# Kernel optimization log

Hardware: AMD Instinct MI355X
Metric: run time of the kernel (lower is better)

Reference implementation:

```python
import jax, jax.numpy as jnp
import numpy as np
from jax import lax

DIM = 96
B, S = 2, 48
EPS_LN = 1e-6
EPS_GRN = 1e-6


def setup_inputs() -> dict:
    key = jax.random.key(0)
    ks = jax.random.split(key, 11)
    d, h = DIM, 4 * DIM
    return {
        "x": jax.random.normal(ks[0], (B, d, S, S, S), jnp.float32),
        "dw_w": jax.random.normal(ks[1], (d, 1, 7, 7, 7), jnp.float32) * 0.05,  # (O, I/groups, kD,kH,kW)
        "dw_b": jax.random.normal(ks[2], (d,), jnp.float32) * 0.02,
        "ln_w": jnp.ones((d,), jnp.float32),
        "ln_b": jnp.zeros((d,), jnp.float32),
        "w1": jax.random.normal(ks[3], (d, h), jnp.float32) * 0.02,
        "b1": jax.random.normal(ks[4], (h,), jnp.float32) * 0.02,
        "grn_w": jax.random.normal(ks[5], (h,), jnp.float32) * 0.02,
        "grn_b": jax.random.normal(ks[6], (h,), jnp.float32) * 0.02,
        "w2": jax.random.normal(ks[7], (h, d), jnp.float32) * 0.02,
        "b2": jax.random.normal(ks[8], (d,), jnp.float32) * 0.02,
    }


def reference(x, dw_w, dw_b, ln_w, ln_b, w1, b1, grn_w, grn_b, w2, b2):
    # depthwise 7x7x7 conv, padding 3, groups = channels; x: (B, C, D, H, W)
    y = lax.conv_general_dilated(
        x, dw_w, window_strides=(1, 1, 1), padding=[(3, 3)] * 3,
        dimension_numbers=("NCDHW", "OIDHW", "NCDHW"), feature_group_count=DIM,
    ) + dw_b[None, :, None, None, None]
    # channels_last: (B, D, H, W, C)
    h = jnp.transpose(y, (0, 2, 3, 4, 1))
    # LayerNorm over channel dim
    mu = jnp.mean(h, axis=-1, keepdims=True)
    var = jnp.mean((h - mu) ** 2, axis=-1, keepdims=True)
    h = (h - mu) * lax.rsqrt(var + EPS_LN) * ln_w + ln_b
    # pointwise MLP expand + GELU (exact, erf-based, like torch)
    h = jnp.einsum("bdhwc,ce->bdhwe", h, w1) + b1
    h = jax.nn.gelu(h, approximate=False)
    # GRN: global L2 norm over spatial dims (1,2,3), per channel
    g = jnp.sqrt(jnp.sum(h * h, axis=(1, 2, 3), keepdims=True))  # (B,1,1,1,4C)
    n = g / (jnp.mean(g, axis=-1, keepdims=True) + EPS_GRN)
    h = grn_w * (h * n) + grn_b + h
    # pointwise MLP contract
    h = jnp.einsum("bdhwe,ec->bdhwc", h, w2) + b2
    # back to channels_first + residual
    return x + jnp.transpose(h, (0, 4, 1, 2, 3))
```

## Files before the change

### kernel.cpp

```cpp
#include <hip/hip_runtime.h>
#include <hip/hip_bf16.h>
#include <string.h>

#define S3 110592
#define CDIM 96
#define EDIM 384
#define ZIN 14
#define YIN 22

typedef __attribute__((ext_vector_type(8))) short bf16x8;
typedef __attribute__((ext_vector_type(4))) float f32x4;
typedef unsigned short ushort_t;

__device__ __forceinline__ ushort_t f2bf(float f) {
  __hip_bfloat16 h = __float2bfloat16(f);
  union { __hip_bfloat16 h; ushort_t u; } cv; cv.h = h; return cv.u;
}
__device__ __forceinline__ float bf2f(ushort_t u) {
  union { __hip_bfloat16 h; ushort_t u; } cv; cv.u = u; return __bfloat162float(cv.h);
}

__global__ void kprep(const float* __restrict__ ln_w, const float* __restrict__ ln_b,
                      const float* __restrict__ w1, const float* __restrict__ b1,
                      const float* __restrict__ grn_b, const float* __restrict__ w2,
                      const float* __restrict__ b2,
                      ushort_t* __restrict__ w1p, float* __restrict__ b1f, float* __restrict__ bias2) {
  int idx = blockIdx.x * 256 + threadIdx.x;
  if (idx < 24 * 3 * 64 * 8) {
    int j = idx & 7, lane = (idx >> 3) & 63, ks = (idx >> 9) % 3, nt = idx / 1536;
    int c = ks * 32 + (lane >> 4) * 8 + j;
    int e = nt * 16 + (lane & 15);
    w1p[idx] = f2bf(ln_w[c] * w1[c * EDIM + e]);
  }
  if (idx < EDIM) {
    float s = b1[idx];
    for (int c = 0; c < CDIM; ++c) s += ln_b[c] * w1[c * EDIM + idx];
    b1f[idx] = s;
  }
  if (idx < CDIM) {
    float s = b2[idx];
    for (int e = 0; e < EDIM; ++e) s += grn_b[e] * w2[e * CDIM + idx];
    bias2[idx] = s;
  }
}

__global__ void kpackB(const float* __restrict__ dw_w, ushort_t* __restrict__ Btab) {
  int idx = blockIdx.x * 256 + threadIdx.x;
  if (idx >= 96 * 49 * 512) return;
  int pos = idx & 511; int t = (idx >> 9) % 49; int c = idx / (49 * 512);
  int lane = pos >> 3, j = pos & 7;
  int k = (lane >> 4) * 8 + j, n = lane & 15;
  int tx = k - n - 1;
  int tz = t / 7, ty = t % 7;
  float v = (tx >= 0 && tx < 7) ? dw_w[c * 343 + tz * 49 + ty * 7 + tx] : 0.f;
  Btab[idx] = f2bf(v);
}

template<int HALF>
__device__ __forceinline__ void conv_ty_loop(const unsigned* tile, const ushort_t* Bt,
                                             int lane, int am, int xg, f32x4* acc) {
#pragma unroll 1
  for (int ty = 0; ty < 7; ++ty) {
    bf16x8 bfr[7];
#pragma unroll
    for (int tz = 0; tz < 7; ++tz)
      bfr[tz] = *(const bf16x8*)&Bt[(tz * 7 + ty) * 512 + lane * 8];
    int rowbase = am + ty;
#pragma unroll
    for (int zl = 0; zl < 7; ++zl) {
      int row = (HALF * 7 + zl) * YIN + rowbase;
      int byteoff = (row << 7) + (xg ^ ((row & 7) << 4));
      bf16x8 af = *(const bf16x8*)((const char*)tile + byteoff);
#pragma unroll
      for (int tz = 0; tz < 7; ++tz) {
        int l = (HALF == 0) ? (zl - tz) : (zl + 6 - tz);
        if (l >= 0 && l < 7)
          acc[l] = __builtin_amdgcn_mfma_f32_16x16x32_bf16(af, bfr[tz], acc[l], 0, 0, 0);
      }
    }
  }
}

__global__ __launch_bounds__(384, 6) void kconv(const float* __restrict__ x,
                                                const ushort_t* __restrict__ Btab,
                                                const float* __restrict__ dw_b,
                                                ushort_t* __restrict__ y) {
  __shared__ unsigned tile[ZIN * YIN * 32];
  int bid = blockIdx.x;
  int yt = bid % 3, zt = (bid / 3) % 6, bc = bid / 18;
  int c = bc % 96;
  int z0 = zt * 8, y0 = yt * 16;
  size_t base = (size_t)bc * S3;
  int tid = threadIdx.x;

  for (int i = tid; i < 308 * 8; i += 384) {
    int row = i >> 3; int pe = i & 7;
    int pc = (pe < 2) ? pe : pe + 24;
    tile[(row << 5) + (pc ^ ((row & 7) << 2))] = 0u;
  }
#pragma unroll 4
  for (int i = tid; i < 308 * 24; i += 384) {
    int row = i / 24; int pc = 2 + (i - row * 24);
    int dz = row / YIN, dy = row - dz * YIN;
    int gz = z0 - 3 + dz, gy = y0 - 3 + dy;
    float2 v = make_float2(0.f, 0.f);
    if ((unsigned)gz < 48u && (unsigned)gy < 48u)
      v = *(const float2*)&x[base + (size_t)gz * 2304 + gy * 48 + 2 * pc - 4];
    tile[(row << 5) + (pc ^ ((row & 7) << 2))] = (unsigned)f2bf(v.x) | ((unsigned)f2bf(v.y) << 16);
  }
  __syncthreads();

  int w = tid >> 6;
  int X = w % 3, half = w / 3;
  int lane = tid & 63;
  int am = lane & 15, g = lane >> 4;
  int xg = X * 32 + g * 16;

  f32x4 acc[7];
#pragma unroll
  for (int p = 0; p < 7; ++p) acc[p] = (f32x4){0.f, 0.f, 0.f, 0.f};

  const ushort_t* __restrict__ Bt = Btab + (size_t)c * 49 * 512;
  if (half == 0) conv_ty_loop<0>(tile, Bt, lane, am, xg, acc);
  else           conv_ty_loop<1>(tile, Bt, lane, am, xg, acc);

  float bv = dw_b[c];
  float* red = (float*)tile;
  int rcol = X * 16 + am;
  __syncthreads();
  if (half == 0) {
#pragma unroll
    for (int l = 1; l < 7; ++l)
#pragma unroll
      for (int r = 0; r < 4; ++r)
        red[(l - 1) * 800 + (g * 4 + r) * 50 + rcol] = acc[l][r];
  }
  __syncthreads();
  if (half == 0) {
    size_t zb = base + (size_t)z0 * 2304;
#pragma unroll
    for (int r = 0; r < 4; ++r)
      y[zb + (size_t)(y0 + g * 4 + r) * 48 + rcol] = f2bf(acc[0][r] + bv);
  } else {
#pragma unroll
    for (int l = 0; l < 7; ++l) {
      size_t zb = base + (size_t)(z0 + l + 1) * 2304;
#pragma unroll
      for (int r = 0; r < 4; ++r) {
        float v = acc[l][r] + bv;
        if (l < 6) v += red[l * 800 + (g * 4 + r) * 50 + rcol];
        y[zb + (size_t)(y0 + g * 4 + r) * 48 + rcol] = f2bf(v);
      }
    }
  }
}

__global__ __launch_bounds__(512, 4) void kmlp1(const ushort_t* __restrict__ y,
                                                const ushort_t* __restrict__ w1p,
                                                const float* __restrict__ b1f,
                                                ushort_t* __restrict__ h,
                                                float* __restrict__ sumsq) {
  __shared__ ushort_t Al[64 * 104];
  __shared__ float red_s[8][64], red_q[8][64];
  __shared__ float stat_mu[64], stat_rv[64];
  int tid = threadIdx.x;
  int q = tid >> 6, lane = tid & 63;
  size_t pos0 = (size_t)blockIdx.x * 64;
  int b = (int)(pos0 / S3);
  int sp0 = (int)(pos0 % S3);

  float v[12];
  float s = 0.f, ss = 0.f;
  const ushort_t* yb = y + (size_t)b * 96 * S3 + sp0 + lane;
#pragma unroll
  for (int i = 0; i < 12; ++i) {
    float f = bf2f(yb[(size_t)(q * 12 + i) * S3]);
    v[i] = f; s += f; ss += f * f;
  }
  red_s[q][lane] = s; red_q[q][lane] = ss;
  __syncthreads();
  if (tid < 64) {
    float su = 0.f, sq = 0.f;
#pragma unroll
    for (int k = 0; k < 8; ++k) { su += red_s[k][tid]; sq += red_q[k][tid]; }
    float mu = su * (1.f / 96.f);
    float var = sq * (1.f / 96.f) - mu * mu;
    stat_mu[tid] = mu;
    stat_rv[tid] = rsqrtf(var + 1e-6f);
  }
  __syncthreads();
  {
    float mu = stat_mu[lane], rv = stat_rv[lane];
#pragma unroll
    for (int i4 = 0; i4 < 3; ++i4) {
      ushort_t u0 = f2bf((v[i4 * 4 + 0] - mu) * rv);
      ushort_t u1 = f2bf((v[i4 * 4 + 1] - mu) * rv);
      ushort_t u2 = f2bf((v[i4 * 4 + 2] - mu) * rv);
      ushort_t u3 = f2bf((v[i4 * 4 + 3] - mu) * rv);
      uint2 t; t.x = (unsigned)u0 | ((unsigned)u1 << 16); t.y = (unsigned)u2 | ((unsigned)u3 << 16);
      *(uint2*)&Al[lane * 104 + q * 12 + i4 * 4] = t;
    }
  }
  __syncthreads();

  f32x4 acc[4][3];
#pragma unroll
  for (int mt = 0; mt < 4; ++mt)
#pragma unroll
    for (int ntl = 0; ntl < 3; ++ntl) acc[mt][ntl] = (f32x4){0.f, 0.f, 0.f, 0.f};

  int row = lane & 15, g = lane >> 4;
#pragma unroll
  for (int ks = 0; ks < 3; ++ks) {
    bf16x8 af[4];
    int colb = ks * 32 + g * 8;
#pragma unroll
    for (int mt = 0; mt < 4; ++mt)
      af[mt] = *(const bf16x8*)&Al[(mt * 16 + row) * 104 + colb];
#pragma unroll
    for (int ntl = 0; ntl < 3; ++ntl) {
      bf16x8 bfg = *(const bf16x8*)&w1p[(size_t)(((q * 3 + ntl) * 3 + ks) * 64 + lane) * 8];
#pragma unroll
      for (int mt = 0; mt < 4; ++mt)
        acc[mt][ntl] = __builtin_amdgcn_mfma_f32_16x16x32_bf16(af[mt], bfg, acc[mt][ntl], 0, 0, 0);
    }
  }

#pragma unroll
  for (int ntl = 0; ntl < 3; ++ntl) {
    int e = q * 48 + ntl * 16 + row;
    float bb = b1f[e];
    float ssq = 0.f;
#pragma unroll
    for (int mt = 0; mt < 4; ++mt) {
#pragma unroll
      for (int r = 0; r < 4; ++r) {
        float val = acc[mt][ntl][r] + bb;
        float gel = 0.5f * val * (1.f + erff(val * 0.70710678118f));
        size_t p = pos0 + mt * 16 + g * 4 + r;
        h[p * EDIM + e] = f2bf(gel);
        ssq += gel * gel;
      }
    }
    ssq += __shfl_xor(ssq, 16, 64);
    ssq += __shfl_xor(ssq, 32, 64);
    if (g == 0) atomicAdd(&sumsq[b * EDIM + e], ssq);
  }
}

__global__ void kscale(const float* __restrict__ sumsq, const float* __restrict__ grn_w,
                       float* __restrict__ scale) {
  __shared__ float wsum[6];
  __shared__ float mean_s;
  int b = blockIdx.x, e = threadIdx.x;
  float gv = sqrtf(sumsq[b * EDIM + e]);
  float t = gv;
#pragma unroll
  for (int off = 1; off <= 32; off <<= 1) t += __shfl_xor(t, off, 64);
  if ((e & 63) == 0) wsum[e >> 6] = t;
  __syncthreads();
  if (e == 0) {
    float m = 0.f;
    for (int i = 0; i < 6; ++i) m += wsum[i];
    mean_s = m * (1.f / EDIM);
  }
  __syncthreads();
  scale[b * EDIM + e] = grn_w[e] * (gv / (mean_s + 1e-6f)) + 1.f;
}

__global__ void kpackw2(const float* __restrict__ scale, const float* __restrict__ w2,
                        ushort_t* __restrict__ w2s) {
  int idx = blockIdx.x * 256 + threadIdx.x;
  int b = idx / 36864; int r = idx % 36864;
  int j = r & 7, lane = (r >> 3) & 63, ks = (r >> 9) % 12, nt = r / 6144;
  int e = ks * 32 + (lane >> 4) * 8 + j, cc = nt * 16 + (lane & 15);
  w2s[idx] = f2bf(scale[b * EDIM + e] * w2[e * CDIM + cc]);
}

__global__ __launch_bounds__(256, 4) void kmlp2(const ushort_t* __restrict__ h,
                                                const ushort_t* __restrict__ w2s,
                                                const float* __restrict__ bias2,
                                                const float* __restrict__ x,
                                                float* __restrict__ out) {
  __shared__ float tile[96 * 65];
  int tid = threadIdx.x;
  int w = tid >> 6, lane = tid & 63;
  size_t pos0 = (size_t)blockIdx.x * 64;
  int b = (int)(pos0 / S3);
  int sp0 = (int)(pos0 % S3);
  int row = lane & 15, g = lane >> 4;

  f32x4 acc[6];
#pragma unroll
  for (int nt = 0; nt < 6; ++nt) acc[nt] = (f32x4){0.f, 0.f, 0.f, 0.f};

  const ushort_t* w2b = w2s + (size_t)b * 36864;
  size_t abase = (pos0 + w * 16 + row) * (size_t)EDIM + g * 8;
#pragma unroll
  for (int ks = 0; ks < 12; ++ks) {
    bf16x8 af = *(const bf16x8*)&h[abase + ks * 32];
#pragma unroll
    for (int nt = 0; nt < 6; ++nt) {
      bf16x8 bfg = *(const bf16x8*)&w2b[(size_t)((nt * 12 + ks) * 64 + lane) * 8];
      acc[nt] = __builtin_amdgcn_mfma_f32_16x16x32_bf16(af, bfg, acc[nt], 0, 0, 0);
    }
  }

#pragma unroll
  for (int nt = 0; nt < 6; ++nt) {
    int cc = nt * 16 + row;
#pragma unroll
    for (int r = 0; r < 4; ++r)
      tile[cc * 65 + w * 16 + g * 4 + r] = acc[nt][r];
  }
  __syncthreads();
#pragma unroll
  for (int k = 0; k < 12; ++k) {
    int idx = tid + k * 256;
    int cc = idx >> 5, pp = (idx & 31) * 2;
    size_t o = (size_t)(b * 96 + cc) * S3 + sp0 + pp;
    float2 xv = *(const float2*)&x[o];
    float bb = bias2[cc];
    float2 ov;
    ov.x = xv.x + tile[cc * 65 + pp] + bb;
    ov.y = xv.y + tile[cc * 65 + pp + 1] + bb;
    *(float2*)&out[o] = ov;
  }
}

extern "C" void kernel_launch(void* const* d_in, const int* in_sizes, int n_in,
                              void* d_out, int out_size, void* d_ws, size_t ws_size,
                              hipStream_t stream) {
  const float* x     = (const float*)d_in[0];
  const float* dw_w  = (const float*)d_in[1];
  const float* dw_b  = (const float*)d_in[2];
  const float* ln_w  = (const float*)d_in[3];
  const float* ln_b  = (const float*)d_in[4];
  const float* w1    = (const float*)d_in[5];
  const float* b1    = (const float*)d_in[6];
  const float* grn_w = (const float*)d_in[7];
  const float* grn_b = (const float*)d_in[8];
  const float* w2    = (const float*)d_in[9];
  const float* b2    = (const float*)d_in[10];
  float* out = (float*)d_out;

  char* ws = (char*)d_ws;
  size_t off = 0;
  auto alloc = [&](size_t bytes) -> void* {
    void* p = ws + off;
    off = (off + bytes + 511) & ~(size_t)511;
    return p;
  };
  ushort_t* y    = (ushort_t*)alloc((size_t)2 * 96 * S3 * 2);
  ushort_t* h    = (ushort_t*)alloc((size_t)221184 * EDIM * 2);
  ushort_t* w1p  = (ushort_t*)alloc(36864 * 2);
  ushort_t* w2s  = (ushort_t*)alloc((size_t)2 * 36864 * 2);
  ushort_t* Btab = (ushort_t*)alloc((size_t)96 * 49 * 512 * 2);
  float* b1f     = (float*)alloc(EDIM * 4);
  float* bias2   = (float*)alloc(CDIM * 4);
  float* sumsq   = (float*)alloc(2 * EDIM * 4);
  float* scale   = (float*)alloc(2 * EDIM * 4);

  hipMemsetAsync(sumsq, 0, 2 * EDIM * 4, stream);
  kprep<<<145, 256, 0, stream>>>(ln_w, ln_b, w1, b1, grn_b, w2, b2, w1p, b1f, bias2);
  kpackB<<<9408, 256, 0, stream>>>(dw_w, Btab);
  kconv<<<3456, 384, 0, stream>>>(x, Btab, dw_b, y);
  kmlp1<<<3456, 512, 0, stream>>>(y, w1p, b1f, h, sumsq);
  kscale<<<2, 384, 0, stream>>>(sumsq, grn_w, scale);
  kpackw2<<<288, 256, 0, stream>>>(scale, w2, w2s);
  kmlp2<<<3456, 256, 0, stream>>>(h, w2s, bias2, x, out);
}
```

Before: 348.0 us.

## Retile depthwise conv, stage weights in LDS, batch atomics, widen MLP2 tile

The conv kernel now uses 16x16 z-y tiles with 768 threads. The tap weights are staged in shared memory, and each wave computes 4 independent z-slices, so the cross-half reduction through shared memory is gone. The block-index mapping groups channels per XCD for cache locality. kmlp1 preloads its w1 fragments into registers and reduces its sum-of-squares atomics to one per channel per block. kmlp2 processes 128 positions per block so each w2 fragment load feeds two MFMAs. The larger tiles cost more halo and shared memory, more registers, and lower occupancy.

```diff
diff --git a/kernel.cpp b/kernel.cpp
--- a/kernel.cpp
+++ b/kernel.cpp
@@ -5,8 +5,6 @@
 #define S3 110592
 #define CDIM 96
 #define EDIM 384
-#define ZIN 14
-#define YIN 22
 
 typedef __attribute__((ext_vector_type(8))) short bf16x8;
 typedef __attribute__((ext_vector_type(4))) float f32x4;
@@ -56,102 +54,82 @@
   Btab[idx] = f2bf(v);
 }
 
-template<int HALF>
-__device__ __forceinline__ void conv_ty_loop(const unsigned* tile, const ushort_t* Bt,
-                                             int lane, int am, int xg, f32x4* acc) {
-#pragma unroll 1
-  for (int ty = 0; ty < 7; ++ty) {
-    bf16x8 bfr[7];
-#pragma unroll
-    for (int tz = 0; tz < 7; ++tz)
-      bfr[tz] = *(const bf16x8*)&Bt[(tz * 7 + ty) * 512 + lane * 8];
-    int rowbase = am + ty;
-#pragma unroll
-    for (int zl = 0; zl < 7; ++zl) {
-      int row = (HALF * 7 + zl) * YIN + rowbase;
-      int byteoff = (row << 7) + (xg ^ ((row & 7) << 4));
-      bf16x8 af = *(const bf16x8*)((const char*)tile + byteoff);
-#pragma unroll
-      for (int tz = 0; tz < 7; ++tz) {
-        int l = (HALF == 0) ? (zl - tz) : (zl + 6 - tz);
-        if (l >= 0 && l < 7)
-          acc[l] = __builtin_amdgcn_mfma_f32_16x16x32_bf16(af, bfr[tz], acc[l], 0, 0, 0);
-      }
-    }
-  }
-}
-
-__global__ __launch_bounds__(384, 6) void kconv(const float* __restrict__ x,
+__global__ __launch_bounds__(768, 3) void kconv(const float* __restrict__ x,
                                                 const ushort_t* __restrict__ Btab,
                                                 const float* __restrict__ dw_b,
                                                 ushort_t* __restrict__ y) {
-  __shared__ unsigned tile[ZIN * YIN * 32];
+  __shared__ unsigned sh[22 * 22 * 32 + 12544];
+  unsigned* tile = sh;
+  ushort_t* btl = (ushort_t*)(sh + 15488);
+  int tid = threadIdx.x;
+
   int bid = blockIdx.x;
-  int yt = bid % 3, zt = (bid / 3) % 6, bc = bid / 18;
-  int c = bc % 96;
-  int z0 = zt * 8, y0 = yt * 16;
-  size_t base = (size_t)bc * S3;
-  int tid = threadIdx.x;
-
-  for (int i = tid; i < 308 * 8; i += 384) {
+  int xcd = bid & 7, wi = bid >> 3;
+  int c = xcd * 12 + wi / 18;
+  int rr_ = wi % 18;
+  int b = rr_ / 9, zt = (rr_ % 9) / 3, yt = rr_ % 3;
+  int z0 = zt * 16, y0 = yt * 16;
+  size_t base = (size_t)(b * 96 + c) * S3;
+
+  for (int i = tid; i < 484 * 8; i += 768) {
     int row = i >> 3; int pe = i & 7;
     int pc = (pe < 2) ? pe : pe + 24;
     tile[(row << 5) + (pc ^ ((row & 7) << 2))] = 0u;
   }
-#pragma unroll 4
-  for (int i = tid; i < 308 * 24; i += 384) {
+  for (int i = tid; i < 484 * 24; i += 768) {
     int row = i / 24; int pc = 2 + (i - row * 24);
-    int dz = row / YIN, dy = row - dz * YIN;
+    int dz = row / 22, dy = row - dz * 22;
     int gz = z0 - 3 + dz, gy = y0 - 3 + dy;
     float2 v = make_float2(0.f, 0.f);
     if ((unsigned)gz < 48u && (unsigned)gy < 48u)
       v = *(const float2*)&x[base + (size_t)gz * 2304 + gy * 48 + 2 * pc - 4];
     tile[(row << 5) + (pc ^ ((row & 7) << 2))] = (unsigned)f2bf(v.x) | ((unsigned)f2bf(v.y) << 16);
   }
+  {
+    uint4* d4 = (uint4*)btl;
+    const uint4* s4 = (const uint4*)(Btab + (size_t)c * 49 * 512);
+    for (int i = tid; i < 3136; i += 768) d4[i] = s4[i];
+  }
   __syncthreads();
 
   int w = tid >> 6;
-  int X = w % 3, half = w / 3;
+  int X = w % 3, Q = w / 3;
   int lane = tid & 63;
   int am = lane & 15, g = lane >> 4;
   int xg = X * 32 + g * 16;
 
-  f32x4 acc[7];
-#pragma unroll
-  for (int p = 0; p < 7; ++p) acc[p] = (f32x4){0.f, 0.f, 0.f, 0.f};
-
-  const ushort_t* __restrict__ Bt = Btab + (size_t)c * 49 * 512;
-  if (half == 0) conv_ty_loop<0>(tile, Bt, lane, am, xg, acc);
-  else           conv_ty_loop<1>(tile, Bt, lane, am, xg, acc);
+  f32x4 acc[4];
+#pragma unroll
+  for (int p = 0; p < 4; ++p) acc[p] = (f32x4){0.f, 0.f, 0.f, 0.f};
+
+#pragma unroll 1
+  for (int ty = 0; ty < 7; ++ty) {
+    bf16x8 bfr[7];
+#pragma unroll
+    for (int tz = 0; tz < 7; ++tz)
+      bfr[tz] = *(const bf16x8*)&btl[(tz * 7 + ty) * 512 + lane * 8];
+    int rowbase = am + ty;
+#pragma unroll
+    for (int zl = 0; zl < 10; ++zl) {
+      int row = (Q * 4 + zl) * 22 + rowbase;
+      int byteoff = (row << 7) + (xg ^ ((row & 7) << 4));
+      bf16x8 af = *(const bf16x8*)((const char*)tile + byteoff);
+#pragma unroll
+      for (int tz = 0; tz < 7; ++tz) {
+        int l = zl - tz;
+        if (l >= 0 && l < 4)
+          acc[l] = __builtin_amdgcn_mfma_f32_16x16x32_bf16(af, bfr[tz], acc[l], 0, 0, 0);
+      }
+    }
+  }
 
   float bv = dw_b[c];
-  float* red = (float*)tile;
-  int rcol = X * 16 + am;
-  __syncthreads();
-  if (half == 0) {
-#pragma unroll
-    for (int l = 1; l < 7; ++l)
-#pragma unroll
-      for (int r = 0; r < 4; ++r)
-        red[(l - 1) * 800 + (g * 4 + r) * 50 + rcol] = acc[l][r];
-  }
-  __syncthreads();
-  if (half == 0) {
-    size_t zb = base + (size_t)z0 * 2304;
+#pragma unroll
+  for (int l = 0; l < 4; ++l) {
+    size_t zb = base + (size_t)(z0 + Q * 4 + l) * 2304;
 #pragma unroll
     for (int r = 0; r < 4; ++r)
-      y[zb + (size_t)(y0 + g * 4 + r) * 48 + rcol] = f2bf(acc[0][r] + bv);
-  } else {
-#pragma unroll
-    for (int l = 0; l < 7; ++l) {
-      size_t zb = base + (size_t)(z0 + l + 1) * 2304;
-#pragma unroll
-      for (int r = 0; r < 4; ++r) {
-        float v = acc[l][r] + bv;
-        if (l < 6) v += red[l * 800 + (g * 4 + r) * 50 + rcol];
-        y[zb + (size_t)(y0 + g * 4 + r) * 48 + rcol] = f2bf(v);
-      }
-    }
+      y[zb + (size_t)(y0 + g * 4 + r) * 48 + X * 16 + am] = f2bf(acc[l][r] + bv);
   }
 }
 
@@ -163,11 +141,19 @@
   __shared__ ushort_t Al[64 * 104];
   __shared__ float red_s[8][64], red_q[8][64];
   __shared__ float stat_mu[64], stat_rv[64];
+  __shared__ float ssq_s[EDIM];
   int tid = threadIdx.x;
   int q = tid >> 6, lane = tid & 63;
   size_t pos0 = (size_t)blockIdx.x * 64;
   int b = (int)(pos0 / S3);
   int sp0 = (int)(pos0 % S3);
+
+  bf16x8 bfg[3][3];
+#pragma unroll
+  for (int ntl = 0; ntl < 3; ++ntl)
+#pragma unroll
+    for (int ks = 0; ks < 3; ++ks)
+      bfg[ntl][ks] = *(const bf16x8*)&w1p[(size_t)(((q * 3 + ntl) * 3 + ks) * 64 + lane) * 8];
 
   float v[12];
   float s = 0.f, ss = 0.f;
@@ -219,10 +205,9 @@
       af[mt] = *(const bf16x8*)&Al[(mt * 16 + row) * 104 + colb];
 #pragma unroll
     for (int ntl = 0; ntl < 3; ++ntl) {
-      bf16x8 bfg = *(const bf16x8*)&w1p[(size_t)(((q * 3 + ntl) * 3 + ks) * 64 + lane) * 8];
 #pragma unroll
       for (int mt = 0; mt < 4; ++mt)
-        acc[mt][ntl] = __builtin_amdgcn_mfma_f32_16x16x32_bf16(af[mt], bfg, acc[mt][ntl], 0, 0, 0);
+        acc[mt][ntl] = __builtin_amdgcn_mfma_f32_16x16x32_bf16(af[mt], bfg[ntl][ks], acc[mt][ntl], 0, 0, 0);
     }
   }
 
@@ -244,8 +229,10 @@
     }
     ssq += __shfl_xor(ssq, 16, 64);
     ssq += __shfl_xor(ssq, 32, 64);
-    if (g == 0) atomicAdd(&sumsq[b * EDIM + e], ssq);
-  }
+    if (g == 0) ssq_s[e] = ssq;
+  }
+  __syncthreads();
+  if (tid < EDIM) atomicAdd(&sumsq[b * EDIM + tid], ssq_s[tid]);
 }
 
 __global__ void kscale(const float* __restrict__ sumsq, const float* __restrict__ grn_w,
@@ -285,46 +272,55 @@
   __shared__ float tile[96 * 65];
   int tid = threadIdx.x;
   int w = tid >> 6, lane = tid & 63;
-  size_t pos0 = (size_t)blockIdx.x * 64;
+  size_t pos0 = (size_t)blockIdx.x * 128;
   int b = (int)(pos0 / S3);
   int sp0 = (int)(pos0 % S3);
   int row = lane & 15, g = lane >> 4;
 
-  f32x4 acc[6];
-#pragma unroll
-  for (int nt = 0; nt < 6; ++nt) acc[nt] = (f32x4){0.f, 0.f, 0.f, 0.f};
+  f32x4 acc[2][6];
+#pragma unroll
+  for (int hf = 0; hf < 2; ++hf)
+#pragma unroll
+    for (int nt = 0; nt < 6; ++nt) acc[hf][nt] = (f32x4){0.f, 0.f, 0.f, 0.f};
 
   const ushort_t* w2b = w2s + (size_t)b * 36864;
-  size_t abase = (pos0 + w * 16 + row) * (size_t)EDIM + g * 8;
+  size_t abase0 = (pos0 + w * 16 + row) * (size_t)EDIM + g * 8;
+  size_t abase1 = abase0 + (size_t)64 * EDIM;
 #pragma unroll
   for (int ks = 0; ks < 12; ++ks) {
-    bf16x8 af = *(const bf16x8*)&h[abase + ks * 32];
+    bf16x8 af0 = *(const bf16x8*)&h[abase0 + ks * 32];
+    bf16x8 af1 = *(const bf16x8*)&h[abase1 + ks * 32];
 #pragma unroll
     for (int nt = 0; nt < 6; ++nt) {
       bf16x8 bfg = *(const bf16x8*)&w2b[(size_t)((nt * 12 + ks) * 64 + lane) * 8];
-      acc[nt] = __builtin_amdgcn_mfma_f32_16x16x32_bf16(af, bfg, acc[nt], 0, 0, 0);
-    }
-  }
-
-#pragma unroll
-  for (int nt = 0; nt < 6; ++nt) {
-    int cc = nt * 16 + row;
-#pragma unroll
-    for (int r = 0; r < 4; ++r)
-      tile[cc * 65 + w * 16 + g * 4 + r] = acc[nt][r];
-  }
-  __syncthreads();
-#pragma unroll
-  for (int k = 0; k < 12; ++k) {
-    int idx = tid + k * 256;
-    int cc = idx >> 5, pp = (idx & 31) * 2;
-    size_t o = (size_t)(b * 96 + cc) * S3 + sp0 + pp;
-    float2 xv = *(const float2*)&x[o];
-    float bb = bias2[cc];
-    float2 ov;
-    ov.x = xv.x + tile[cc * 65 + pp] + bb;
-    ov.y = xv.y + tile[cc * 65 + pp + 1] + bb;
-    *(float2*)&out[o] = ov;
+      acc[0][nt] = __builtin_amdgcn_mfma_f32_16x16x32_bf16(af0, bfg, acc[0][nt], 0, 0, 0);
+      acc[1][nt] = __builtin_amdgcn_mfma_f32_16x16x32_bf16(af1, bfg, acc[1][nt], 0, 0, 0);
+    }
+  }
+
+#pragma unroll
+  for (int hf = 0; hf < 2; ++hf) {
+    __syncthreads();
+#pragma unroll
+    for (int nt = 0; nt < 6; ++nt) {
+      int cc = nt * 16 + row;
+#pragma unroll
+      for (int r = 0; r < 4; ++r)
+        tile[cc * 65 + w * 16 + g * 4 + r] = acc[hf][nt][r];
+    }
+    __syncthreads();
+#pragma unroll
+    for (int k = 0; k < 12; ++k) {
+      int idx = tid + k * 256;
+      int cc = idx >> 5, pp = (idx & 31) * 2;
+      size_t o = (size_t)(b * 96 + cc) * S3 + sp0 + hf * 64 + pp;
+      float2 xv = *(const float2*)&x[o];
+      float bb = bias2[cc];
+      float2 ov;
+      ov.x = xv.x + tile[cc * 65 + pp] + bb;
+      ov.y = xv.y + tile[cc * 65 + pp + 1] + bb;
+      *(float2*)&out[o] = ov;
+    }
   }
 }
 
@@ -364,9 +360,9 @@
   hipMemsetAsync(sumsq, 0, 2 * EDIM * 4, stream);
   kprep<<<145, 256, 0, stream>>>(ln_w, ln_b, w1, b1, grn_b, w2, b2, w1p, b1f, bias2);
   kpackB<<<9408, 256, 0, stream>>>(dw_w, Btab);
-  kconv<<<3456, 384, 0, stream>>>(x, Btab, dw_b, y);
+  kconv<<<1728, 768, 0, stream>>>(x, Btab, dw_b, y);
   kmlp1<<<3456, 512, 0, stream>>>(y, w1p, b1f, h, sumsq);
   kscale<<<2, 384, 0, stream>>>(sumsq, grn_w, scale);
   kpackw2<<<288, 256, 0, stream>>>(scale, w2, w2s);
-  kmlp2<<<3456, 256, 0, stream>>>(h, w2s, bias2, x, out);
-}
+  kmlp2<<<1728, 256, 0, stream>>>(h, w2s, bias2, x, out);
+}
```

Measured after the change: 339.1 us. 1.03x faster.

## Remap conv blocks per XCD, preload W1 fragments, batch GRN atomics, double MLP2 tile

Applied to the files above, without the earlier changes.

The conv kernel's block index is remapped so that each XCD (blocks grouped by bid&7) handles a contiguous set of channels, which should improve L2 reuse of per-channel weight tables. kmlp1 loads all W1 fragments into registers up front and gathers per-channel sum-of-squares in shared memory, so each block issues one atomic per channel instead of one per wave. kmlp2 now processes 128 positions per block, reusing each W2 fragment load across two MFMA row tiles and halving the grid. These changes raise register pressure and add extra syncs in the mlp2 epilogue.

```diff
diff --git a/kernel.cpp b/kernel.cpp
--- a/kernel.cpp
+++ b/kernel.cpp
@@ -87,10 +87,14 @@
                                                 ushort_t* __restrict__ y) {
   __shared__ unsigned tile[ZIN * YIN * 32];
   int bid = blockIdx.x;
-  int yt = bid % 3, zt = (bid / 3) % 6, bc = bid / 18;
-  int c = bc % 96;
+  int xcd = bid & 7, wi = bid >> 3;
+  int c = xcd * 12 + wi / 36;
+  int rr_ = wi % 36;
+  int b = rr_ / 18;
+  int t_ = rr_ % 18;
+  int zt = t_ / 3, yt = t_ % 3;
   int z0 = zt * 8, y0 = yt * 16;
-  size_t base = (size_t)bc * S3;
+  size_t base = (size_t)(b * 96 + c) * S3;
   int tid = threadIdx.x;
 
   for (int i = tid; i < 308 * 8; i += 384) {
@@ -163,11 +167,19 @@
   __shared__ ushort_t Al[64 * 104];
   __shared__ float red_s[8][64], red_q[8][64];
   __shared__ float stat_mu[64], stat_rv[64];
+  __shared__ float ssq_s[EDIM];
   int tid = threadIdx.x;
   int q = tid >> 6, lane = tid & 63;
   size_t pos0 = (size_t)blockIdx.x * 64;
   int b = (int)(pos0 / S3);
   int sp0 = (int)(pos0 % S3);
+
+  bf16x8 bfg[3][3];
+#pragma unroll
+  for (int ntl = 0; ntl < 3; ++ntl)
+#pragma unroll
+    for (int ks = 0; ks < 3; ++ks)
+      bfg[ntl][ks] = *(const bf16x8*)&w1p[(size_t)(((q * 3 + ntl) * 3 + ks) * 64 + lane) * 8];
 
   float v[12];
   float s = 0.f, ss = 0.f;
@@ -219,10 +231,9 @@
       af[mt] = *(const bf16x8*)&Al[(mt * 16 + row) * 104 + colb];
 #pragma unroll
     for (int ntl = 0; ntl < 3; ++ntl) {
-      bf16x8 bfg = *(const bf16x8*)&w1p[(size_t)(((q * 3 + ntl) * 3 + ks) * 64 + lane) * 8];
 #pragma unroll
       for (int mt = 0; mt < 4; ++mt)
-        acc[mt][ntl] = __builtin_amdgcn_mfma_f32_16x16x32_bf16(af[mt], bfg, acc[mt][ntl], 0, 0, 0);
+        acc[mt][ntl] = __builtin_amdgcn_mfma_f32_16x16x32_bf16(af[mt], bfg[ntl][ks], acc[mt][ntl], 0, 0, 0);
     }
   }
 
@@ -244,8 +255,10 @@
     }
     ssq += __shfl_xor(ssq, 16, 64);
     ssq += __shfl_xor(ssq, 32, 64);
-    if (g == 0) atomicAdd(&sumsq[b * EDIM + e], ssq);
-  }
+    if (g == 0) ssq_s[e] = ssq;
+  }
+  __syncthreads();
+  if (tid < EDIM) atomicAdd(&sumsq[b * EDIM + tid], ssq_s[tid]);
 }
 
 __global__ void kscale(const float* __restrict__ sumsq, const float* __restrict__ grn_w,
@@ -285,46 +298,55 @@
   __shared__ float tile[96 * 65];
   int tid = threadIdx.x;
   int w = tid >> 6, lane = tid & 63;
-  size_t pos0 = (size_t)blockIdx.x * 64;
+  size_t pos0 = (size_t)blockIdx.x * 128;
   int b = (int)(pos0 / S3);
   int sp0 = (int)(pos0 % S3);
   int row = lane & 15, g = lane >> 4;
 
-  f32x4 acc[6];
-#pragma unroll
-  for (int nt = 0; nt < 6; ++nt) acc[nt] = (f32x4){0.f, 0.f, 0.f, 0.f};
+  f32x4 acc[2][6];
+#pragma unroll
+  for (int hf = 0; hf < 2; ++hf)
+#pragma unroll
+    for (int nt = 0; nt < 6; ++nt) acc[hf][nt] = (f32x4){0.f, 0.f, 0.f, 0.f};
 
   const ushort_t* w2b = w2s + (size_t)b * 36864;
-  size_t abase = (pos0 + w * 16 + row) * (size_t)EDIM + g * 8;
+  size_t abase0 = (pos0 + w * 16 + row) * (size_t)EDIM + g * 8;
+  size_t abase1 = abase0 + (size_t)64 * EDIM;
 #pragma unroll
   for (int ks = 0; ks < 12; ++ks) {
-    bf16x8 af = *(const bf16x8*)&h[abase + ks * 32];
+    bf16x8 af0 = *(const bf16x8*)&h[abase0 + ks * 32];
+    bf16x8 af1 = *(const bf16x8*)&h[abase1 + ks * 32];
 #pragma unroll
     for (int nt = 0; nt < 6; ++nt) {
       bf16x8 bfg = *(const bf16x8*)&w2b[(size_t)((nt * 12 + ks) * 64 + lane) * 8];
-      acc[nt] = __builtin_amdgcn_mfma_f32_16x16x32_bf16(af, bfg, acc[nt], 0, 0, 0);
-    }
-  }
-
-#pragma unroll
-  for (int nt = 0; nt < 6; ++nt) {
-    int cc = nt * 16 + row;
-#pragma unroll
-    for (int r = 0; r < 4; ++r)
-      tile[cc * 65 + w * 16 + g * 4 + r] = acc[nt][r];
-  }
-  __syncthreads();
-#pragma unroll
-  for (int k = 0; k < 12; ++k) {
-    int idx = tid + k * 256;
-    int cc = idx >> 5, pp = (idx & 31) * 2;
-    size_t o = (size_t)(b * 96 + cc) * S3 + sp0 + pp;
-    float2 xv = *(const float2*)&x[o];
-    float bb = bias2[cc];
-    float2 ov;
-    ov.x = xv.x + tile[cc * 65 + pp] + bb;
-    ov.y = xv.y + tile[cc * 65 + pp + 1] + bb;
-    *(float2*)&out[o] = ov;
+      acc[0][nt] = __builtin_amdgcn_mfma_f32_16x16x32_bf16(af0, bfg, acc[0][nt], 0, 0, 0);
+      acc[1][nt] = __builtin_amdgcn_mfma_f32_16x16x32_bf16(af1, bfg, acc[1][nt], 0, 0, 0);
+    }
+  }
+
+#pragma unroll
+  for (int hf = 0; hf < 2; ++hf) {
+    __syncthreads();
+#pragma unroll
+    for (int nt = 0; nt < 6; ++nt) {
+      int cc = nt * 16 + row;
+#pragma unroll
+      for (int r = 0; r < 4; ++r)
+        tile[cc * 65 + w * 16 + g * 4 + r] = acc[hf][nt][r];
+    }
+    __syncthreads();
+#pragma unroll
+    for (int k = 0; k < 12; ++k) {
+      int idx = tid + k * 256;
+      int cc = idx >> 5, pp = (idx & 31) * 2;
+      size_t o = (size_t)(b * 96 + cc) * S3 + sp0 + hf * 64 + pp;
+      float2 xv = *(const float2*)&x[o];
+      float bb = bias2[cc];
+      float2 ov;
+      ov.x = xv.x + tile[cc * 65 + pp] + bb;
+      ov.y = xv.y + tile[cc * 65 + pp + 1] + bb;
+      *(float2*)&out[o] = ov;
+    }
   }
 }
 
@@ -368,5 +390,5 @@
   kmlp1<<<3456, 512, 0, stream>>>(y, w1p, b1f, h, sumsq);
   kscale<<<2, 384, 0, stream>>>(sumsq, grn_w, scale);
   kpackw2<<<288, 256, 0, stream>>>(scale, w2, w2s);
-  kmlp2<<<3456, 256, 0, stream>>>(h, w2s, bias2, x, out);
-}
+  kmlp2<<<1728, 256, 0, stream>>>(h, w2s, bias2, x, out);
+}
```

After: 337.7 us. 1.03x faster.
